# Kernel tuning notes

Measured on AMD Instinct MI355X. Metric: run time of the kernel, lower is better.

## Reference

```python
import jax, jax.numpy as jnp
import numpy as np
import math

B, S, D, H = 2, 4096, 768, 12
HD = D // H            # 64
BLK = 32               # MRA block size (hard-coded in the module)
NBR = S // BLK         # 128 blocks per row
NUM_BLOCK = 1024       # selected score blocks per (batch*head)
APPROX_MODE = "full"
FIRST_N = 0            # initial_prior_first_n_blocks
DIAG_N = 3             # initial_prior_diagonal_n_blocks
MB = B * H


def setup_inputs() -> dict:
    key = jax.random.key(0)
    ks = jax.random.split(key, 4)
    scale = 0.02
    return {
        "X": jax.random.normal(ks[0], (B, S, D), jnp.float32),
        "mask": jnp.ones((B, S), jnp.float32),
        "Wq": scale * jax.random.normal(ks[1], (D, D), jnp.float32),
        "bq": jnp.zeros((D,), jnp.float32),
        "Wk": scale * jax.random.normal(ks[2], (D, D), jnp.float32),
        "bk": jnp.zeros((D,), jnp.float32),
        "Wv": scale * jax.random.normal(ks[3], (D, D), jnp.float32),
        "bv": jnp.zeros((D,), jnp.float32),
    }


def _mra2_attention(Q, K, V, mask):
    # Q, K, V: [MB, S, HD]; mask: [MB, S] (float 0/1)
    inv_sqrt_d = 1.0 / math.sqrt(HD)
    Q = Q * mask[:, :, None]
    K = K * mask[:, :, None]
    V = V * mask[:, :, None]

    # ---- low-resolution (block-mean) logits ----
    token_count = mask.reshape(MB, NBR, BLK).sum(-1)                 # [MB, NBR]
    denom = token_count[:, :, None] + 1e-6
    Qh = Q.reshape(MB, NBR, BLK, HD).sum(2) / denom                  # [MB, NBR, HD]
    Kh = K.reshape(MB, NBR, BLK, HD).sum(2) / denom
    Vh = V.reshape(MB, NBR, BLK, HD).sum(2) / denom

    low_logit = jnp.einsum('bnd,bmd->bnm', Qh, Kh) * inv_sqrt_d      # [MB, NBR, NBR]
    row_max = low_logit.max(-1, keepdims=True)                        # [MB, NBR, 1] (before empty-pair masking)
    pair_empty = (token_count[:, None, :] * token_count[:, :, None]) < 0.5
    low_logit = low_logit - 1e4 * pair_empty.astype(low_logit.dtype)

    # ---- top-k block selection (no grad) ----
    prior = jax.lax.stop_gradient(low_logit - row_max)
    if DIAG_N > 0:
        off = DIAG_N // 2
        i = jnp.arange(NBR)
        band = (jnp.abs(i[:, None] - i[None, :]) <= off).astype(prior.dtype)
        prior = prior + band[None] * 5e3
    if FIRST_N > 0:
        prior = prior.at[:, :FIRST_N, :].add(5e3)
        prior = prior.at[:, :, :FIRST_N].add(5e3)
    top_vals, indices = jax.lax.top_k(prior.reshape(MB, -1), NUM_BLOCK)  # row-major flat idx = q_blk*NBR + k_blk
    threshold = top_vals.min(-1)
    selected_mask = (prior >= threshold[:, None, None]).astype(jnp.float32)  # 1 for selected low-res blocks

    rblk = indices // NBR   # query block index, [MB, NUM_BLOCK]
    cblk = indices % NBR    # key block index
    bidx = jnp.arange(MB)[:, None]

    Qb = Q.reshape(MB, NBR, BLK, HD)
    Kb = K.reshape(MB, NBR, BLK, HD)
    Vb = V.reshape(MB, NBR, BLK, HD)
    kmask = mask.reshape(MB, NBR, BLK)[bidx, cblk]                   # [MB, NB, 32k]

    Qg = Qb[bidx, rblk]                                              # [MB, NB, 32, HD]
    Kg = Kb[bidx, cblk]
    Vg = Vb[bidx, cblk]

    # ---- high-resolution sparse block logits ----
    logit = jnp.einsum('bnqd,bnkd->bnqk', Qg, Kg) * inv_sqrt_d       # [MB, NB, 32q, 32k]

    seg = (jnp.arange(MB)[:, None] * NBR + rblk).reshape(-1)         # segment id per block -> query row block
    blk_qmax = logit.max(-1).reshape(MB * NUM_BLOCK, BLK)            # per-query-token max within block
    max_rows = jax.ops.segment_max(blk_qmax, seg, num_segments=MB * NBR)
    max_rows = jnp.maximum(max_rows, -1e6).reshape(MB, NBR, BLK)     # guard rows w/o selected blocks
    max_vals = max_rows.reshape(MB, S)                               # per-token sparse row max
    max_scatter = max_rows[bidx, rblk]                               # [MB, NB, 32q]

    logit = logit - max_scatter[:, :, :, None]
    logit = logit - 1e4 * (1.0 - kmask[:, :, None, :])
    attn = jnp.exp(logit)

    blk_out = jnp.einsum('bnqk,bnkd->bnqd', attn, Vg)                # [MB, NB, 32, HD]
    high_out = jax.ops.segment_sum(
        blk_out.reshape(MB * NUM_BLOCK, BLK, HD), seg, num_segments=MB * NBR
    ).reshape(MB, S, HD)
    high_norm = jax.ops.segment_sum(
        attn.sum(-1).reshape(MB * NUM_BLOCK, BLK), seg, num_segments=MB * NBR
    ).reshape(MB, S)

    if APPROX_MODE == "full":
        # low-res attention over NON-selected blocks, weighted by token counts
        low_attn = jnp.exp(low_logit - row_max - 1e4 * selected_mask) * token_count[:, None, :]
        low_out = jnp.einsum('bnm,bmd->bnd', low_attn, Vh)           # [MB, NBR, HD]
        low_out = jnp.repeat(low_out[:, :, None, :], BLK, axis=2).reshape(MB, S, HD)
        low_norm = jnp.repeat(low_attn.sum(-1)[:, :, None], BLK, axis=2).reshape(MB, S)

        log_corr = jnp.repeat(row_max, BLK, axis=2).reshape(MB, S) - max_vals
        log_corr = log_corr * mask
        low_corr = jnp.exp(jnp.minimum(log_corr, 0.0))
        high_corr = jnp.exp(-jnp.maximum(log_corr, 0.0))

        out = (high_out * high_corr[:, :, None] + low_out * low_corr[:, :, None]) / (
            (high_norm * high_corr + low_norm * low_corr + 1e-6)[:, :, None]
        )
    else:  # "sparse"
        out = high_out / (high_norm[:, :, None] + 1e-6)
    return out


def reference(X, mask, Wq, bq, Wk, bk, Wv, bv):
    def proj(W, b):
        y = jnp.einsum('bsd,ed->bse', X, W) + b                       # nn.Linear: x @ W.T + b
        return y.reshape(B, S, H, HD).transpose(0, 2, 1, 3).reshape(MB, S, HD)

    Q, K, V = proj(Wq, bq), proj(Wk, bk), proj(Wv, bv)
    m = jnp.broadcast_to(mask[:, None, :], (B, H, S)).reshape(MB, S)
    out = _mra2_attention(Q, K, V, m)
    return out.reshape(B, H, S, HD).transpose(0, 2, 1, 3).reshape(B, S, D)
```

## Files before the change

### kernel.cpp

```cpp
#include <hip/hip_runtime.h>

typedef __bf16 bf16;
typedef float f32x4 __attribute__((ext_vector_type(4)));
typedef bf16 bf16x8 __attribute__((ext_vector_type(8)));
typedef bf16 bf16x4 __attribute__((ext_vector_type(4)));
typedef unsigned int uint;
typedef unsigned short ushort;


__device__ __forceinline__ void llds16(const bf16* g, bf16* l) {
    __builtin_amdgcn_global_load_lds((const __attribute__((address_space(1))) uint*)g,
                                     (__attribute__((address_space(3))) uint*)l, 16, 0, 0);
}

__device__ __forceinline__ uint sortable(float f) {
    uint u = __float_as_uint(f);
    return u ^ (uint)(((int)u >> 31) | 0x80000000);
}

__global__ __launch_bounds__(256)
void k_prep(const float* __restrict__ X, const float* __restrict__ mask,
            const float* __restrict__ Wq, const float* __restrict__ Wk,
            const float* __restrict__ Wv,
            bf16* __restrict__ Xb, float* __restrict__ Xh, float* __restrict__ tc,
            bf16* __restrict__ Wb) {
    const int p = blockIdx.x;
    const int t = threadIdx.x;
    if (p >= 768) {
        int i = (p - 768) * 256 + t;
        if (i >= 442368) return;
        int n = (i << 2) / 768;
        int k = (i << 2) % 768;
        const float* W = n < 768 ? Wq : (n < 1536 ? Wk : Wv);
        int nn = n - (n < 768 ? 0 : (n < 1536 ? 768 : 1536));
        float4 f = *(const float4*)(W + (size_t)nn * 768 + k);
        bf16x4 o = {(bf16)f.x, (bf16)f.y, (bf16)f.z, (bf16)f.w};
        ((bf16x4*)Wb)[i] = o;
        return;
    }
    const int row = p % 256;
    const int g = p / 256;
    const int b = row >> 7, nbr = row & 127;
    const int c = t & 63;
    const int tq = t >> 6;
    const int c4 = g * 64 + c;
    const size_t base = (size_t)(b * 4096 + nbr * 32) * 768;
    const float4* xp = (const float4*)(X + base) + c4;
    bf16x4* xbp = (bf16x4*)(Xb + base) + c4;
    const float* mp = mask + b * 4096 + nbr * 32;
    __shared__ float4 red[4][64];
    __shared__ float tcr[4];
    float4 s = {0.f, 0.f, 0.f, 0.f};
    float tcs = 0.f;
#pragma unroll
    for (int j = 0; j < 8; ++j) {
        const int tok = tq * 8 + j;
        float4 v = xp[(size_t)tok * 192];
        float m = mp[tok];
        s.x += v.x * m; s.y += v.y * m; s.z += v.z * m; s.w += v.w * m;
        tcs += m;
        bf16x4 o = {(bf16)v.x, (bf16)v.y, (bf16)v.z, (bf16)v.w};
        xbp[(size_t)tok * 192] = o;
    }
    red[tq][c] = s;
    if (c == 0) tcr[tq] = tcs;
    __syncthreads();
    if (tq == 0) {
        float4 a = red[0][c], b2 = red[1][c], c2 = red[2][c], d2 = red[3][c];
        float4 o = {a.x + b2.x + c2.x + d2.x, a.y + b2.y + c2.y + d2.y,
                    a.z + b2.z + c2.z + d2.z, a.w + b2.w + c2.w + d2.w};
        ((float4*)(Xh + (size_t)row * 768))[c4] = o;
        if (c == 0 && g == 0) tc[row] = tcr[0] + tcr[1] + tcr[2] + tcr[3];
    }
}

__global__ __launch_bounds__(256, 4)
void k_gemm_qkv(const bf16* __restrict__ Xb, const bf16* __restrict__ Wb,
                const float* __restrict__ bq, const float* __restrict__ bk,
                const float* __restrict__ bv, const float* __restrict__ mask,
                bf16* __restrict__ Qb, bf16* __restrict__ Kb, bf16* __restrict__ Vt) {
    __shared__ bf16 smem[17408];
    bf16* As = smem;
    bf16* Bs = smem + 8192;
    const int tid = threadIdx.x;
    const int wave = tid >> 6, lane = tid & 63;
    const int quad = lane >> 4, l16 = lane & 15;
    const int wr = wave >> 1, wc = wave & 1;
    const int m0 = blockIdx.x * 128, n0 = blockIdx.y * 128;
    const int srow = lane >> 3;
    const int sgcol = (((lane & 7) ^ (srow & 7)) << 3);

    f32x4 acc[4][4] = {};

    for (int k0 = 0; k0 < 768; k0 += 64) {
        __syncthreads();
#pragma unroll
        for (int it = 0; it < 4; ++it) {
            int R = wave * 32 + it * 8;
            llds16(Xb + (size_t)(m0 + R + srow) * 768 + k0 + sgcol, &As[R * 64]);
            llds16(Wb + (size_t)(n0 + R + srow) * 768 + k0 + sgcol, &Bs[R * 64]);
        }
        __syncthreads();
#pragma unroll
        for (int ks = 0; ks < 2; ++ks) {
            const int pg = ((ks * 4 + quad) ^ (l16 & 7)) << 3;
            bf16x8 a[4], b[4];
#pragma unroll
            for (int i = 0; i < 4; ++i)
                a[i] = *(const bf16x8*)&As[(wr * 64 + i * 16 + l16) * 64 + pg];
#pragma unroll
            for (int i = 0; i < 4; ++i)
                b[i] = *(const bf16x8*)&Bs[(wc * 64 + i * 16 + l16) * 64 + pg];
#pragma unroll
            for (int i = 0; i < 4; ++i)
#pragma unroll
                for (int j = 0; j < 4; ++j)
                    acc[i][j] = __builtin_amdgcn_mfma_f32_16x16x32_bf16(a[i], b[j], acc[i][j], 0, 0, 0);
        }
    }

    const int which = n0 / 768;
    const float* bias = which == 0 ? bq : (which == 1 ? bk : bv);

    __syncthreads();
#pragma unroll
    for (int i = 0; i < 4; ++i) {
        const int rloc0 = wr * 64 + i * 16 + quad * 4;
#pragma unroll
        for (int j = 0; j < 4; ++j) {
            const int cloc = wc * 64 + j * 16 + l16;
            const int hcol = n0 - which * 768 + cloc;
            const float bv_ = bias[hcol];
#pragma unroll
            for (int r = 0; r < 4; ++r) {
                const int rloc = rloc0 + r;
                const int mm = m0 + rloc;
                const int bidx = mm >> 12, s = mm & 4095;
                const float y = (acc[i][j][r] + bv_) * mask[(bidx << 12) + s];
                if (which == 2) smem[cloc * 136 + rloc] = (bf16)y;
                else            smem[rloc * 136 + cloc] = (bf16)y;
            }
        }
    }
    __syncthreads();
    if (which < 2) {
        bf16* dst = which == 0 ? Qb : Kb;
#pragma unroll
        for (int it = 0; it < 8; ++it) {
            const int gidx = it * 256 + tid;
            const int sr = gidx >> 4, chunk = gidx & 15;
            const int mm = m0 + sr;
            const int bidx = mm >> 12, s = mm & 4095;
            const int hcol = n0 - which * 768 + chunk * 8;
            const int h = hcol >> 6, d0 = hcol & 63;
            bf16x8 v = *(const bf16x8*)&smem[sr * 136 + chunk * 8];
            *(bf16x8*)(dst + ((((size_t)(bidx * 12 + h)) << 12) + s) * 64 + d0) = v;
        }
    } else {
#pragma unroll
        for (int it = 0; it < 8; ++it) {
            const int gidx = it * 256 + tid;
            const int drow = gidx >> 4, chunk = gidx & 15;
            const int s0 = chunk * 8;
            const int mm = m0 + s0;
            const int bidx = mm >> 12, s = mm & 4095;
            const int hcol = n0 - 1536 + drow;
            const int h = hcol >> 6, dd = hcol & 63;
            bf16x8 v = *(const bf16x8*)&smem[drow * 136 + s0];
            *(bf16x8*)(Vt + ((((size_t)(bidx * 12 + h)) * 128 + (s >> 5)) * 64 + dd) * 32 + (s & 31)) = v;
        }
    }
}

__global__ __launch_bounds__(256)
void k_lowres_p(const float* __restrict__ Xh,
                const float* __restrict__ Wq, const float* __restrict__ Wk,
                const float* __restrict__ Wv, float* __restrict__ partial) {
    const int nb = blockIdx.x;
    const int rowbase = blockIdx.y * 128;
    const int bz = blockIdx.z;
    const int kb = bz * 112;
    const int klen = (bz == 6) ? 96 : 112;
    const int t = threadIdx.x;

    __shared__ float As[16 * 132];
    __shared__ float Bs[16 * 132];

    const int which = nb / 6;
    const float* Wsel = which == 0 ? Wq : (which == 1 ? Wk : Wv);
    const float* Wbase = Wsel + (size_t)((nb % 6) * 128) * 768;

    const int sr = t >> 2;
    const int skq = t & 3;
    const int tr = t >> 4, tc2 = t & 15;
    const int r0 = tr * 8, c0 = tc2 * 8;

    float acc[8][8] = {};
    float4 va[2], vb[2];
    const int stages = klen >> 4;

#pragma unroll
    for (int i = 0; i < 2; ++i) {
        va[i] = *(const float4*)(Xh + (size_t)(rowbase + sr + 64 * i) * 768 + kb + skq * 4);
        vb[i] = *(const float4*)(Wbase + (size_t)(sr + 64 * i) * 768 + kb + skq * 4);
    }

    for (int s = 0; s < stages; ++s) {
        __syncthreads();
#pragma unroll
        for (int i = 0; i < 2; ++i) {
            const int r = sr + 64 * i;
            As[(skq * 4 + 0) * 132 + r] = va[i].x;
            As[(skq * 4 + 1) * 132 + r] = va[i].y;
            As[(skq * 4 + 2) * 132 + r] = va[i].z;
            As[(skq * 4 + 3) * 132 + r] = va[i].w;
            Bs[(skq * 4 + 0) * 132 + r] = vb[i].x;
            Bs[(skq * 4 + 1) * 132 + r] = vb[i].y;
            Bs[(skq * 4 + 2) * 132 + r] = vb[i].z;
            Bs[(skq * 4 + 3) * 132 + r] = vb[i].w;
        }
        if (s + 1 < stages) {
            const int kc = kb + (s + 1) * 16;
#pragma unroll
            for (int i = 0; i < 2; ++i) {
                va[i] = *(const float4*)(Xh + (size_t)(rowbase + sr + 64 * i) * 768 + kc + skq * 4);
                vb[i] = *(const float4*)(Wbase + (size_t)(sr + 64 * i) * 768 + kc + skq * 4);
            }
        }
        __syncthreads();
#pragma unroll
        for (int k = 0; k < 16; ++k) {
            float4 a0 = *(const float4*)&As[k * 132 + r0];
            float4 a1 = *(const float4*)&As[k * 132 + r0 + 4];
            float4 b0 = *(const float4*)&Bs[k * 132 + c0];
            float4 b1 = *(const float4*)&Bs[k * 132 + c0 + 4];
            float av[8] = {a0.x, a0.y, a0.z, a0.w, a1.x, a1.y, a1.z, a1.w};
            float bv[8] = {b0.x, b0.y, b0.z, b0.w, b1.x, b1.y, b1.z, b1.w};
#pragma unroll
            for (int i = 0; i < 8; ++i)
#pragma unroll
                for (int j = 0; j < 8; ++j)
                    acc[i][j] += av[i] * bv[j];
        }
    }

    float* pp = partial + (size_t)bz * 589824 + (size_t)(rowbase + r0) * 2304 + nb * 128 + c0;
#pragma unroll
    for (int i = 0; i < 8; ++i) {
        float4 s0 = {acc[i][0], acc[i][1], acc[i][2], acc[i][3]};
        float4 s1 = {acc[i][4], acc[i][5], acc[i][6], acc[i][7]};
        *(float4*)(pp + (size_t)i * 2304) = s0;
        *(float4*)(pp + (size_t)i * 2304 + 4) = s1;
    }
}

__global__ __launch_bounds__(256)
void k_lowfin(const float* __restrict__ partial, const float* __restrict__ tc,
              const float* __restrict__ bq, const float* __restrict__ bk,
              const float* __restrict__ bv,
              float* __restrict__ Qh, float* __restrict__ Kh, float* __restrict__ Vh) {
    const int gx = blockIdx.x;
    const int row = blockIdx.y;
    const int t = threadIdx.x;
    const int gcol = gx * 256 + t;
    float s = 0.f;
#pragma unroll
    for (int ch = 0; ch < 7; ++ch)
        s += partial[(size_t)ch * 589824 + (size_t)row * 2304 + gcol];
    const int which = gx / 3;
    const int wcol = (gx % 3) * 256 + t;
    const float* bias = which == 0 ? bq : (which == 1 ? bk : bv);
    const float tcv = tc[row];
    const float val = (s + tcv * bias[wcol]) / (tcv + 1e-6f);
    const int b = row >> 7, nbr = row & 127;
    const int h = wcol >> 6, d = wcol & 63;
    float* dst = which == 0 ? Qh : (which == 1 ? Kh : Vh);
    dst[(((size_t)(b * 12 + h)) * 128 + nbr) * 64 + d] = val;
}

__global__ __launch_bounds__(256)
void k_lowlogit(const float* __restrict__ Qh, const float* __restrict__ Kh,
                float* __restrict__ prior, float* __restrict__ rowmax) {
    int mb = blockIdx.x, rc = blockIdx.y;
    int tid = threadIdx.x;
    __shared__ float Ksh[64 * 132];
    __shared__ float Qsh[16 * 64];
    for (int idx = tid; idx < 128 * 64; idx += 256) {
        int c = idx >> 6, k = idx & 63;
        Ksh[k * 132 + c] = Kh[((size_t)mb * 128 + c) * 64 + k];
    }
    for (int idx = tid; idx < 16 * 64; idx += 256) {
        int r = idx >> 6, k = idx & 63;
        Qsh[idx] = Qh[((size_t)mb * 128 + rc * 16 + r) * 64 + k];
    }
    __syncthreads();
    int rloc = tid >> 4, cg = tid & 15;
    float acc[8] = {};
    for (int k = 0; k < 64; ++k) {
        float qv = Qsh[rloc * 64 + k];
        const float* kr = &Ksh[k * 132 + cg * 8];
#pragma unroll
        for (int j = 0; j < 8; ++j) acc[j] += qv * kr[j];
    }
    float pm = -3.4e38f;
#pragma unroll
    for (int j = 0; j < 8; ++j) { acc[j] *= 0.125f; pm = fmaxf(pm, acc[j]); }
#pragma unroll
    for (int d = 1; d < 16; d <<= 1) pm = fmaxf(pm, __shfl_xor(pm, d, 64));
    int r = rc * 16 + rloc;
    if (cg == 0) rowmax[mb * 128 + r] = pm;
    float* dst = prior + ((size_t)mb * 128 + r) * 128 + cg * 8;
#pragma unroll
    for (int j = 0; j < 8; ++j) dst[j] = acc[j] - pm;
}

__global__ __launch_bounds__(1024)
void k_select(const float* __restrict__ prior, unsigned char* __restrict__ selmask,
              unsigned short* __restrict__ lists, int* __restrict__ counts,
              ushort* __restrict__ qorder) {
    const int mb = blockIdx.x, tid = threadIdx.x;
    const int ln = tid & 63;
    __shared__ int lc[16 * 3];
    __shared__ int cnt[128];
    if (tid < 48) lc[tid] = 0;
    if (tid < 128) cnt[tid] = 0;

    const int r = tid >> 3;
    const int cbase = (tid & 7) << 4;
    uint key[16];
    const float4* P4 = (const float4*)(prior + (size_t)mb * 16384) + (tid << 2);
#pragma unroll
    for (int j4 = 0; j4 < 4; ++j4) {
        float4 v = P4[j4];
        float vv[4] = {v.x, v.y, v.z, v.w};
#pragma unroll
        for (int e = 0; e < 4; ++e) {
            int c = cbase + (j4 << 2) + e;
            float f = vv[e] + ((r - c <= 1 && c - r <= 1) ? 5e3f : 0.f);
            key[(j4 << 2) + e] = sortable(f);
        }
    }
    __syncthreads();

    uint pfx = 0u;
    int k = 1024;
#pragma unroll
    for (int lvl = 0; lvl < 16; ++lvl) {
        const int sh = 30 - 2 * lvl;
        const uint maskA = (lvl == 0) ? 0u : (0xFFFFFFFFu << (sh + 2));
        int c3 = 0, c2 = 0, c1 = 0;
#pragma unroll
        for (int j = 0; j < 16; ++j) {
            uint x = key[j];
            bool m = ((x ^ pfx) & maskA) == 0u;
            uint f = (x >> sh) & 3u;
            c3 += (m && f == 3u);
            c2 += (m && f == 2u);
            c1 += (m && f == 1u);
        }
#pragma unroll
        for (int d = 1; d < 64; d <<= 1) {
            c3 += __shfl_xor(c3, d, 64);
            c2 += __shfl_xor(c2, d, 64);
            c1 += __shfl_xor(c1, d, 64);
        }
        if (ln == 0) {
            atomicAdd(&lc[lvl * 3 + 0], c3);
            atomicAdd(&lc[lvl * 3 + 1], c2);
            atomicAdd(&lc[lvl * 3 + 2], c1);
        }
        __syncthreads();
        const int C3 = lc[lvl * 3 + 0], C2 = lc[lvl * 3 + 1], C1 = lc[lvl * 3 + 2];
        uint choose;
        if (C3 >= k)                { choose = 3u; }
        else if (C3 + C2 >= k)      { choose = 2u; k -= C3; }
        else if (C3 + C2 + C1 >= k) { choose = 1u; k -= C3 + C2; }
        else                        { choose = 0u; k -= C3 + C2 + C1; }
        pfx |= choose << sh;
    }
    const uint T = pfx;

    uint packed[4] = {0u, 0u, 0u, 0u};
#pragma unroll
    for (int j = 0; j < 16; ++j) {
        if (key[j] >= T) {
            packed[j >> 2] |= 1u << ((j & 3) << 3);
            int pos = atomicAdd(&cnt[r], 1);
            lists[((size_t)mb * 128 + r) * 128 + pos] = (unsigned short)(cbase + j);
        }
    }
    uint4 pk;
    pk.x = packed[0]; pk.y = packed[1]; pk.z = packed[2]; pk.w = packed[3];
    *(uint4*)(selmask + (size_t)mb * 16384 + (size_t)tid * 16) = pk;
    __syncthreads();
    if (tid < 128) {
        const int myc = cnt[tid];
        counts[mb * 128 + tid] = myc;
        int rank = 0;
        for (int j = 0; j < 128; ++j) {
            int cj = cnt[j];
            rank += (cj > myc) || (cj == myc && j < tid);
        }
        qorder[mb * 128 + rank] = (ushort)tid;
    }
}

__global__ __launch_bounds__(64)
void k_high(const bf16* __restrict__ Qb, const bf16* __restrict__ Kb,
            const bf16* __restrict__ Vt, const int* __restrict__ counts,
            const unsigned short* __restrict__ lists, const ushort* __restrict__ qorder,
            const float* __restrict__ rowmax, const float* __restrict__ prior,
            const unsigned char* __restrict__ selmask, const float* __restrict__ tc,
            const float* __restrict__ Vh, const float* __restrict__ mask,
            float* __restrict__ out) {
    const int bid = blockIdx.x;
    const int work = ((bid & 7) * 384) + (bid >> 3);
    const int mb = work >> 7;
    const int q = qorder[mb * 128 + (work & 127)];
    const int lane = threadIdx.x, quad = lane >> 4, l16 = lane & 15;
    __shared__ bf16 Pa[32 * 40];
    __shared__ bf16 Pbs[32 * 40];

    const bf16* Qbase = Qb + ((size_t)mb * 4096 + q * 32) * 64;
    bf16x8 qf[2][2];
#pragma unroll
    for (int mt = 0; mt < 2; ++mt)
#pragma unroll
        for (int ks = 0; ks < 2; ++ks)
            qf[mt][ks] = *(const bf16x8*)(Qbase + (mt * 16 + l16) * 64 + ks * 32 + quad * 8);

    bf16x8 ones;
#pragma unroll
    for (int j = 0; j < 8; ++j) ones[j] = (bf16)1.0f;

    float mxl[2][4];
    f32x4 o[2][4] = {};
    f32x4 lac[2] = {};
#pragma unroll
    for (int mt = 0; mt < 2; ++mt)
#pragma unroll
        for (int r = 0; r < 4; ++r) mxl[mt][r] = -3.4e38f;

    int cntv = counts[mb * 128 + q];
    if (cntv > 128) cntv = 128;
    if (cntv < 1) cntv = 1;
    const uint* lst32 = (const uint*)(lists + ((size_t)mb * 128 + q) * 128);

    const bf16* KB = Kb + (size_t)mb * 4096 * 64;
    const bf16* VB = Vt + (size_t)mb * 128 * 2048;

    int koff[2][2], voff[4];
#pragma unroll
    for (int nt = 0; nt < 2; ++nt)
#pragma unroll
        for (int ks = 0; ks < 2; ++ks) koff[nt][ks] = (nt * 16 + l16) * 64 + ks * 32 + quad * 8;
#pragma unroll
    for (int nd = 0; nd < 4; ++nd) voff[nd] = (nd * 16 + l16) * 32 + quad * 8;

    bf16x8 kA[2][2], vA[4], kB[2][2], vB[4];
    {
        const uint pr = lst32[0];
        const int cA = __builtin_amdgcn_readfirstlane((int)(pr & 0xffffu));
        const bf16* kp = KB + (size_t)cA * 2048;
        const bf16* vp = VB + (size_t)cA * 2048;
#pragma unroll
        for (int nt = 0; nt < 2; ++nt)
#pragma unroll
            for (int ks = 0; ks < 2; ++ks) kA[nt][ks] = *(const bf16x8*)(kp + koff[nt][ks]);
#pragma unroll
        for (int nd = 0; nd < 4; ++nd) vA[nd] = *(const bf16x8*)(vp + voff[nd]);
        if (cntv > 1) {
            const int cB = __builtin_amdgcn_readfirstlane((int)(pr >> 16));
            const bf16* kp2 = KB + (size_t)cB * 2048;
            const bf16* vp2 = VB + (size_t)cB * 2048;
#pragma unroll
            for (int nt = 0; nt < 2; ++nt)
#pragma unroll
                for (int ks = 0; ks < 2; ++ks) kB[nt][ks] = *(const bf16x8*)(kp2 + koff[nt][ks]);
#pragma unroll
            for (int nd = 0; nd < 4; ++nd) vB[nd] = *(const bf16x8*)(vp2 + voff[nd]);
        }
    }

    float lo = 0.f, ln = 0.f;
    {
        const float* pn = prior + ((size_t)mb * 128 + q) * 128;
        const uint* sel32 = (const uint*)(selmask + ((size_t)mb * 128 + q) * 128);
        const float* tcb = tc + (mb / 12) * 128;
        const float* Vb = Vh + (size_t)mb * 128 * 64;
#pragma unroll 4
        for (int c = 0; c < 128; ++c) {
            if (!((sel32[c >> 2] >> ((c & 3) << 3)) & 1u)) {
                float w = __expf(pn[c]) * tcb[c];
                lo += w * Vb[c * 64 + lane];
                ln += w;
            }
        }
    }

    for (int i = 0; i < cntv; i += 2) {
        const bool hasB = (i + 1 < cntv);
        const bool hasAn = (i + 2 < cntv);
        const bool hasBn = (i + 3 < cntv);
        int cAn = 0, cBn = 0;
        if (hasAn) {
            const uint prn = lst32[(i >> 1) + 1];
            cAn = __builtin_amdgcn_readfirstlane((int)(prn & 0xffffu));
            cBn = __builtin_amdgcn_readfirstlane((int)(prn >> 16));
        }

        {
            f32x4 sf[2][2] = {};
            __builtin_amdgcn_s_setprio(1);
#pragma unroll
            for (int mt = 0; mt < 2; ++mt)
#pragma unroll
                for (int nt = 0; nt < 2; ++nt) {
                    sf[mt][nt] = __builtin_amdgcn_mfma_f32_16x16x32_bf16(qf[mt][0], kA[nt][0], sf[mt][nt], 0, 0, 0);
                    sf[mt][nt] = __builtin_amdgcn_mfma_f32_16x16x32_bf16(qf[mt][1], kA[nt][1], sf[mt][nt], 0, 0, 0);
                }
            __builtin_amdgcn_s_setprio(0);
#pragma unroll
            for (int mt = 0; mt < 2; ++mt)
#pragma unroll
                for (int r = 0; r < 4; ++r) {
                    mxl[mt][r] = fmaxf(mxl[mt][r], fmaxf(sf[mt][0][r], sf[mt][1][r]));
                    float e0, e1;
                    asm("v_exp_f32 %0, %1" : "=v"(e0) : "v"(sf[mt][0][r] * 0.18033688011112042f));
                    asm("v_exp_f32 %0, %1" : "=v"(e1) : "v"(sf[mt][1][r] * 0.18033688011112042f));
                    Pa[(mt * 16 + quad * 4 + r) * 40 + l16] = (bf16)e0;
                    Pa[(mt * 16 + quad * 4 + r) * 40 + 16 + l16] = (bf16)e1;
                }
        }
        if (hasB) {
            f32x4 sf[2][2] = {};
            __builtin_amdgcn_s_setprio(1);
#pragma unroll
            for (int mt = 0; mt < 2; ++mt)
#pragma unroll
                for (int nt = 0; nt < 2; ++nt) {
                    sf[mt][nt] = __builtin_amdgcn_mfma_f32_16x16x32_bf16(qf[mt][0], kB[nt][0], sf[mt][nt], 0, 0, 0);
                    sf[mt][nt] = __builtin_amdgcn_mfma_f32_16x16x32_bf16(qf[mt][1], kB[nt][1], sf[mt][nt], 0, 0, 0);
                }
            __builtin_amdgcn_s_setprio(0);
#pragma unroll
            for (int mt = 0; mt < 2; ++mt)
#pragma unroll
                for (int r = 0; r < 4; ++r) {
                    mxl[mt][r] = fmaxf(mxl[mt][r], fmaxf(sf[mt][0][r], sf[mt][1][r]));
                    float e0, e1;
                    asm("v_exp_f32 %0, %1" : "=v"(e0) : "v"(sf[mt][0][r] * 0.18033688011112042f));
                    asm("v_exp_f32 %0, %1" : "=v"(e1) : "v"(sf[mt][1][r] * 0.18033688011112042f));
                    Pbs[(mt * 16 + quad * 4 + r) * 40 + l16] = (bf16)e0;
                    Pbs[(mt * 16 + quad * 4 + r) * 40 + 16 + l16] = (bf16)e1;
                }
        }

        if (hasAn) {
            const bf16* kp = KB + (size_t)cAn * 2048;
#pragma unroll
            for (int nt = 0; nt < 2; ++nt)
#pragma unroll
                for (int ks = 0; ks < 2; ++ks) kA[nt][ks] = *(const bf16x8*)(kp + koff[nt][ks]);
        }
        if (hasBn) {
            const bf16* kp = KB + (size_t)cBn * 2048;
#pragma unroll
            for (int nt = 0; nt < 2; ++nt)
#pragma unroll
                for (int ks = 0; ks < 2; ++ks) kB[nt][ks] = *(const bf16x8*)(kp + koff[nt][ks]);
        }

        asm volatile("s_waitcnt lgkmcnt(0)" ::: "memory");
        bf16x8 pa[2], pb[2];
#pragma unroll
        for (int mt = 0; mt < 2; ++mt)
            pa[mt] = *(const bf16x8*)&Pa[(mt * 16 + l16) * 40 + quad * 8];
        if (hasB) {
#pragma unroll
            for (int mt = 0; mt < 2; ++mt)
                pb[mt] = *(const bf16x8*)&Pbs[(mt * 16 + l16) * 40 + quad * 8];
        }
        __builtin_amdgcn_s_setprio(1);
#pragma unroll
        for (int mt = 0; mt < 2; ++mt) {
#pragma unroll
            for (int nd = 0; nd < 4; ++nd)
                o[mt][nd] = __builtin_amdgcn_mfma_f32_16x16x32_bf16(pa[mt], vA[nd], o[mt][nd], 0, 0, 0);
            lac[mt] = __builtin_amdgcn_mfma_f32_16x16x32_bf16(pa[mt], ones, lac[mt], 0, 0, 0);
        }
        if (hasB) {
#pragma unroll
            for (int mt = 0; mt < 2; ++mt) {
#pragma unroll
                for (int nd = 0; nd < 4; ++nd)
                    o[mt][nd] = __builtin_amdgcn_mfma_f32_16x16x32_bf16(pb[mt], vB[nd], o[mt][nd], 0, 0, 0);
                lac[mt] = __builtin_amdgcn_mfma_f32_16x16x32_bf16(pb[mt], ones, lac[mt], 0, 0, 0);
            }
        }
        __builtin_amdgcn_s_setprio(0);

        if (hasAn) {
            const bf16* vp = VB + (size_t)cAn * 2048;
#pragma unroll
            for (int nd = 0; nd < 4; ++nd) vA[nd] = *(const bf16x8*)(vp + voff[nd]);
        }
        if (hasBn) {
            const bf16* vp = VB + (size_t)cBn * 2048;
#pragma unroll
            for (int nd = 0; nd < 4; ++nd) vB[nd] = *(const bf16x8*)(vp + voff[nd]);
        }
    }

#pragma unroll
    for (int d = 1; d < 16; d <<= 1)
#pragma unroll
        for (int mt = 0; mt < 2; ++mt)
#pragma unroll
            for (int r = 0; r < 4; ++r)
                mxl[mt][r] = fmaxf(mxl[mt][r], __shfl_xor(mxl[mt][r], d, 64));

    const int b = mb / 12, h = mb - b * 12;
    const float rm = rowmax[mb * 128 + q];
#pragma unroll
    for (int mt = 0; mt < 2; ++mt)
#pragma unroll
        for (int r = 0; r < 4; ++r) {
            const int s = q * 32 + mt * 16 + quad * 4 + r;
            const float mv = fmaxf(mxl[mt][r] * 0.125f, -1e6f);
            const float hn = lac[mt][r];
            const float mk = mask[(b << 12) + s];
            const float lcr = (rm - mv) * mk;
            const float lcf = __expf(fminf(lcr, 0.f));
            const float hcf = __expf(-mv - fmaxf(lcr, 0.f));
            const float den = 1.0f / (hn * hcf + ln * lcf + 1e-6f);
            float* op = out + ((size_t)(b * 4096 + s)) * 768 + h * 64;
#pragma unroll
            for (int nd = 0; nd < 4; ++nd) {
                const int d = nd * 16 + l16;
                const float LOd = __shfl(lo, d, 64);
                op[d] = (o[mt][nd][r] * hcf + LOd * lcf) * den;
            }
        }
}

extern "C" void kernel_launch(void* const* d_in, const int* in_sizes, int n_in,
                              void* d_out, int out_size, void* d_ws, size_t ws_size,
                              hipStream_t stream) {
    (void)in_sizes; (void)n_in; (void)out_size; (void)ws_size;
    const float* X    = (const float*)d_in[0];
    const float* mask = (const float*)d_in[1];
    const float* Wq   = (const float*)d_in[2];
    const float* bq   = (const float*)d_in[3];
    const float* Wk   = (const float*)d_in[4];
    const float* bk   = (const float*)d_in[5];
    const float* Wv   = (const float*)d_in[6];
    const float* bv   = (const float*)d_in[7];
    float* out = (float*)d_out;

    char* ws = (char*)d_ws;
    size_t off = 0;
    auto alloc = [&](size_t bytes) -> void* {
        off = (off + 255) & ~(size_t)255;
        void* p = ws + off;
        off += bytes;
        return p;
    };
    bf16* Xb  = (bf16*)alloc((size_t)8192 * 768 * 2);
    bf16* Wb  = (bf16*)alloc((size_t)2304 * 768 * 2);
    bf16* Qb  = (bf16*)alloc((size_t)24 * 4096 * 64 * 2);
    bf16* Kb  = (bf16*)alloc((size_t)24 * 4096 * 64 * 2);
    bf16* Vt  = (bf16*)alloc((size_t)24 * 4096 * 64 * 2);
    float* Xh = (float*)alloc((size_t)256 * 768 * 4);
    float* tc = (float*)alloc(256 * 4);
    float* Qh = (float*)alloc((size_t)24 * 128 * 64 * 4);
    float* Kh = (float*)alloc((size_t)24 * 128 * 64 * 4);
    float* Vh = (float*)alloc((size_t)24 * 128 * 64 * 4);
    float* prior = (float*)alloc((size_t)24 * 16384 * 4);
    float* rowmax = (float*)alloc(24 * 128 * 4);
    unsigned char* selmask = (unsigned char*)alloc((size_t)24 * 16384);
    unsigned short* lists = (unsigned short*)alloc((size_t)24 * 128 * 128 * 2);
    int* counts = (int*)alloc(24 * 128 * 4);
    ushort* qorder = (ushort*)alloc(24 * 128 * 2);
    float* partial   = (float*)alloc((size_t)7 * 589824 * 4);

    k_prep<<<2496, 256, 0, stream>>>(X, mask, Wq, Wk, Wv, Xb, Xh, tc, Wb);
    k_gemm_qkv<<<dim3(64, 18), 256, 0, stream>>>(Xb, Wb, bq, bk, bv, mask, Qb, Kb, Vt);
    k_lowres_p<<<dim3(18, 2, 7), 256, 0, stream>>>(Xh, Wq, Wk, Wv, partial);
    k_lowfin<<<dim3(9, 256), 256, 0, stream>>>(partial, tc, bq, bk, bv, Qh, Kh, Vh);
    k_lowlogit<<<dim3(24, 8), 256, 0, stream>>>(Qh, Kh, prior, rowmax);
    k_select<<<24, 1024, 0, stream>>>(prior, selmask, lists, counts, qorder);
    k_high<<<3072, 64, 0, stream>>>(Qb, Kb, Vt, counts, lists, qorder, rowmax, prior,
                                    selmask, tc, Vh, mask, out);
}
```

Measured before the change: 260.4 us.

## Precompute full low-res attention sums, subtract selected blocks in high kernel

The low-resolution output and normaliser are now computed over all 128 blocks inside k_lowlogit, using a shared-memory weight tile and the block-mean V. k_high starts from these full sums and subtracts the contributions of the selected blocks inside its main loop. This replaces a serial 128-iteration masked loop per work item. The trade-off is extra work in k_lowlogit and possible cancellation error from subtracting large terms in fp32.

```diff
diff --git a/kernel.cpp b/kernel.cpp
--- a/kernel.cpp
+++ b/kernel.cpp
@@ -280,11 +280,14 @@
 
 __global__ __launch_bounds__(256)
 void k_lowlogit(const float* __restrict__ Qh, const float* __restrict__ Kh,
-                float* __restrict__ prior, float* __restrict__ rowmax) {
+                const float* __restrict__ tc, const float* __restrict__ Vh,
+                float* __restrict__ prior, float* __restrict__ rowmax,
+                float* __restrict__ full_lo, float* __restrict__ full_ln) {
     int mb = blockIdx.x, rc = blockIdx.y;
     int tid = threadIdx.x;
     __shared__ float Ksh[64 * 132];
     __shared__ float Qsh[16 * 64];
+    __shared__ float Wsh[16 * 132];
     for (int idx = tid; idx < 128 * 64; idx += 256) {
         int c = idx >> 6, k = idx & 63;
         Ksh[k * 132 + c] = Kh[((size_t)mb * 128 + c) * 64 + k];
@@ -310,8 +313,41 @@
     int r = rc * 16 + rloc;
     if (cg == 0) rowmax[mb * 128 + r] = pm;
     float* dst = prior + ((size_t)mb * 128 + r) * 128 + cg * 8;
-#pragma unroll
-    for (int j = 0; j < 8; ++j) dst[j] = acc[j] - pm;
+    const float* tcb = tc + (mb / 12) * 128;
+    float lnv = 0.f;
+#pragma unroll
+    for (int j = 0; j < 8; ++j) {
+        const float pv = acc[j] - pm;
+        dst[j] = pv;
+        const float w = __expf(pv) * tcb[cg * 8 + j];
+        Wsh[rloc * 132 + cg * 8 + j] = w;
+        lnv += w;
+    }
+#pragma unroll
+    for (int d = 1; d < 16; d <<= 1) lnv += __shfl_xor(lnv, d, 64);
+    if (cg == 0) full_ln[mb * 128 + r] = lnv;
+    __syncthreads();
+    float* Vsh = Ksh;
+    for (int idx = tid; idx < 128 * 64; idx += 256) {
+        int c = idx >> 6, d = idx & 63;
+        Vsh[c * 66 + d] = Vh[((size_t)mb * 128 + c) * 64 + d];
+    }
+    __syncthreads();
+    const int d = tid & 63, grp = tid >> 6;
+    float o0 = 0.f, o1 = 0.f, o2 = 0.f, o3 = 0.f;
+    const float* W0 = &Wsh[(grp * 4 + 0) * 132];
+    const float* W1 = &Wsh[(grp * 4 + 1) * 132];
+    const float* W2 = &Wsh[(grp * 4 + 2) * 132];
+    const float* W3 = &Wsh[(grp * 4 + 3) * 132];
+    for (int c = 0; c < 128; ++c) {
+        const float v = Vsh[c * 66 + d];
+        o0 += W0[c] * v; o1 += W1[c] * v; o2 += W2[c] * v; o3 += W3[c] * v;
+    }
+    const size_t qb = (size_t)mb * 128 + rc * 16 + grp * 4;
+    full_lo[(qb + 0) * 64 + d] = o0;
+    full_lo[(qb + 1) * 64 + d] = o1;
+    full_lo[(qb + 2) * 64 + d] = o2;
+    full_lo[(qb + 3) * 64 + d] = o3;
 }
 
 __global__ __launch_bounds__(1024)
@@ -410,9 +446,9 @@
             const bf16* __restrict__ Vt, const int* __restrict__ counts,
             const unsigned short* __restrict__ lists, const ushort* __restrict__ qorder,
             const float* __restrict__ rowmax, const float* __restrict__ prior,
-            const unsigned char* __restrict__ selmask, const float* __restrict__ tc,
-            const float* __restrict__ Vh, const float* __restrict__ mask,
-            float* __restrict__ out) {
+            const float* __restrict__ tc, const float* __restrict__ Vh,
+            const float* __restrict__ full_lo, const float* __restrict__ full_ln,
+            const float* __restrict__ mask, float* __restrict__ out) {
     const int bid = blockIdx.x;
     const int work = ((bid & 7) * 384) + (bid >> 3);
     const int mb = work >> 7;
@@ -448,6 +484,9 @@
 
     const bf16* KB = Kb + (size_t)mb * 4096 * 64;
     const bf16* VB = Vt + (size_t)mb * 128 * 2048;
+    const float* pn = prior + ((size_t)mb * 128 + q) * 128;
+    const float* tcb = tc + (mb / 12) * 128;
+    const float* VhB = Vh + (size_t)mb * 128 * 64;
 
     int koff[2][2], voff[4];
 #pragma unroll
@@ -456,6 +495,9 @@
         for (int ks = 0; ks < 2; ++ks) koff[nt][ks] = (nt * 16 + l16) * 64 + ks * 32 + quad * 8;
 #pragma unroll
     for (int nd = 0; nd < 4; ++nd) voff[nd] = (nd * 16 + l16) * 32 + quad * 8;
+
+    float lo = full_lo[((size_t)mb * 128 + q) * 64 + lane];
+    float ln = full_ln[mb * 128 + q];
 
     bf16x8 kA[2][2], vA[4], kB[2][2], vB[4];
     {
@@ -479,22 +521,6 @@
                 for (int ks = 0; ks < 2; ++ks) kB[nt][ks] = *(const bf16x8*)(kp2 + koff[nt][ks]);
 #pragma unroll
             for (int nd = 0; nd < 4; ++nd) vB[nd] = *(const bf16x8*)(vp2 + voff[nd]);
-        }
-    }
-
-    float lo = 0.f, ln = 0.f;
-    {
-        const float* pn = prior + ((size_t)mb * 128 + q) * 128;
-        const uint* sel32 = (const uint*)(selmask + ((size_t)mb * 128 + q) * 128);
-        const float* tcb = tc + (mb / 12) * 128;
-        const float* Vb = Vh + (size_t)mb * 128 * 64;
-#pragma unroll 4
-        for (int c = 0; c < 128; ++c) {
-            if (!((sel32[c >> 2] >> ((c & 3) << 3)) & 1u)) {
-                float w = __expf(pn[c]) * tcb[c];
-                lo += w * Vb[c * 64 + lane];
-                ln += w;
-            }
         }
     }
 
@@ -569,6 +595,20 @@
             for (int nt = 0; nt < 2; ++nt)
 #pragma unroll
                 for (int ks = 0; ks < 2; ++ks) kB[nt][ks] = *(const bf16x8*)(kp + koff[nt][ks]);
+        }
+
+        {
+            const uint prc = lst32[i >> 1];
+            const int cAc = (int)(prc & 0xffffu);
+            const float wA = __expf(pn[cAc]) * tcb[cAc];
+            lo -= wA * VhB[cAc * 64 + lane];
+            ln -= wA;
+            if (hasB) {
+                const int cBc = (int)(prc >> 16);
+                const float wB = __expf(pn[cBc]) * tcb[cBc];
+                lo -= wB * VhB[cBc * 64 + lane];
+                ln -= wB;
+            }
         }
 
         asm volatile("s_waitcnt lgkmcnt(0)" ::: "memory");
@@ -682,14 +722,17 @@
     unsigned short* lists = (unsigned short*)alloc((size_t)24 * 128 * 128 * 2);
     int* counts = (int*)alloc(24 * 128 * 4);
     ushort* qorder = (ushort*)alloc(24 * 128 * 2);
+    float* full_lo = (float*)alloc((size_t)24 * 128 * 64 * 4);
+    float* full_ln = (float*)alloc(24 * 128 * 4);
     float* partial   = (float*)alloc((size_t)7 * 589824 * 4);
 
     k_prep<<<2496, 256, 0, stream>>>(X, mask, Wq, Wk, Wv, Xb, Xh, tc, Wb);
     k_gemm_qkv<<<dim3(64, 18), 256, 0, stream>>>(Xb, Wb, bq, bk, bv, mask, Qb, Kb, Vt);
     k_lowres_p<<<dim3(18, 2, 7), 256, 0, stream>>>(Xh, Wq, Wk, Wv, partial);
     k_lowfin<<<dim3(9, 256), 256, 0, stream>>>(partial, tc, bq, bk, bv, Qh, Kh, Vh);
-    k_lowlogit<<<dim3(24, 8), 256, 0, stream>>>(Qh, Kh, prior, rowmax);
+    k_lowlogit<<<dim3(24, 8), 256, 0, stream>>>(Qh, Kh, tc, Vh, prior, rowmax,
+                                                full_lo, full_ln);
     k_select<<<24, 1024, 0, stream>>>(prior, selmask, lists, counts, qorder);
     k_high<<<3072, 64, 0, stream>>>(Qb, Kb, Vt, counts, lists, qorder, rowmax, prior,
-                                    selmask, tc, Vh, mask, out);
-}
+                                    tc, Vh, full_lo, full_ln, mask, out);
+}
```

Measured after the change: 244.1 us. 1.07x faster.
